# Performance work log

Measured on AMD Instinct MI355X. Metric: run time of the kernel, lower is better.

## Reference

```python
import jax, jax.numpy as jnp
import numpy as np

NDIM = 1024
NHEAD = 16
HEAD_DIM = NDIM // NHEAD


def setup_inputs() -> dict:
    key = jax.random.key(0)
    ks = jax.random.split(key, 12)
    B, L, C = 2, 2048, NDIM
    s = 0.02
    return {
        "q": jax.random.normal(ks[0], (B, L, C), jnp.float32),
        "k": jax.random.normal(ks[1], (B, L, C), jnp.float32),
        "v": jax.random.normal(ks[2], (B, L, C), jnp.float32),
        "Wq": jax.random.normal(ks[3], (C, C), jnp.float32) * s,
        "bq": jax.random.normal(ks[4], (C,), jnp.float32) * s,
        "Wk": jax.random.normal(ks[5], (C, C), jnp.float32) * s,
        "bk": jax.random.normal(ks[6], (C,), jnp.float32) * s,
        "Wv": jax.random.normal(ks[7], (C, C), jnp.float32) * s,
        "bv": jax.random.normal(ks[8], (C,), jnp.float32) * s,
        "Wo": jax.random.normal(ks[9], (C, C), jnp.float32) * s,
        "bo": jax.random.normal(ks[10], (C,), jnp.float32) * s,
    }


def reference(q, k, v, Wq, bq, Wk, bk, Wv, bv, Wo, bo):
    B, Lq, C = q.shape
    H, D = NHEAD, HEAD_DIM
    # projections, then split heads: (B, H, L, D)
    qh = (q @ Wq + bq).reshape(B, Lq, H, D).transpose(0, 2, 1, 3)
    kh = (k @ Wk + bk).reshape(B, k.shape[1], H, D).transpose(0, 2, 1, 3)
    vh = (v @ Wv + bv).reshape(B, v.shape[1], H, D).transpose(0, 2, 1, 3)
    scale = 1.0 / jnp.sqrt(jnp.asarray(D, qh.dtype))
    att = jnp.einsum("bhqd,bhkd->bhqk", qh, kh) * scale  # (B,H,Lq,Lk)
    att = jax.nn.softmax(att, axis=-1)  # dropout p=0.0 -> identity
    y = jnp.einsum("bhqk,bhkd->bhqd", att, vh)
    y = y.transpose(0, 2, 1, 3).reshape(B, Lq, C)
    return y @ Wo + bo
```

## Files before the change

### kernel.cpp

```cpp
#include <hip/hip_runtime.h>
#include <math.h>

#define BATCH 2
#define SEQ   2048
#define CDIM  1024
#define NHEAD 16
#define HDIM  64
#define TOKS  (BATCH * SEQ)

typedef __bf16 bf16x8 __attribute__((ext_vector_type(8)));
typedef __bf16 bf16x2 __attribute__((ext_vector_type(2)));
typedef float  f32x4  __attribute__((ext_vector_type(4)));
typedef float  f32x16 __attribute__((ext_vector_type(16)));

#define MFMA16(a, b, c) __builtin_amdgcn_mfma_f32_16x16x32_bf16(a, b, c, 0, 0, 0)
#define MFMA32(a, b, c) __builtin_amdgcn_mfma_f32_32x32x16_bf16(a, b, c, 0, 0, 0)

#define QSCALE 0.1803368801111204f

__device__ __forceinline__ void gload_lds16(const __bf16* g, __bf16* l) {
    __builtin_amdgcn_global_load_lds(
        (const __attribute__((address_space(1))) unsigned int*)g,
        (__attribute__((address_space(3))) unsigned int*)l, 16, 0, 0);
}

__global__ __launch_bounds__(256) void prep_kernel(
    const float* __restrict__ q, const float* __restrict__ k, const float* __restrict__ v,
    __bf16* __restrict__ qo, __bf16* __restrict__ ko, __bf16* __restrict__ vo,
    const float* __restrict__ W0, const float* __restrict__ W1,
    const float* __restrict__ W2, const float* __restrict__ W3,
    __bf16* __restrict__ T0, __bf16* __restrict__ T1,
    __bf16* __restrict__ T2, __bf16* __restrict__ T3)
{
    __shared__ __bf16 Ts[64][72];
    const int bx = blockIdx.x;
    const int tid = threadIdx.x;

    if (bx < 6144) {
        const int t = bx >> 11;
        const size_t i = ((size_t)(bx & 2047) * 256 + tid) * 8;
        const float* s = t == 0 ? q : (t == 1 ? k : v);
        __bf16* d = t == 0 ? qo : (t == 1 ? ko : vo);
        const float4 x = *(const float4*)&s[i];
        const float4 y = *(const float4*)&s[i + 4];
        bf16x8 o;
        o[0] = (__bf16)x.x; o[1] = (__bf16)x.y; o[2] = (__bf16)x.z; o[3] = (__bf16)x.w;
        o[4] = (__bf16)y.x; o[5] = (__bf16)y.y; o[6] = (__bf16)y.z; o[7] = (__bf16)y.w;
        *(bf16x8*)&d[i] = o;
        return;
    }

    const int t  = bx - 6144;
    const int z  = t >> 8;
    const int ry = (t & 255) >> 4;
    const int rx = t & 15;
    const float* W = z == 0 ? W0 : z == 1 ? W1 : z == 2 ? W2 : W3;
    __bf16* T = z == 0 ? T0 : z == 1 ? T1 : z == 2 ? T2 : T3;
    const int rb = ry * 64, cb = rx * 64;
    const int r = tid >> 4;
    const int c4 = (tid & 15) * 4;
#pragma unroll
    for (int p = 0; p < 4; p++) {
        const int rr = p * 16 + r;
        const float4 w4 = *(const float4*)&W[(size_t)(rb + rr) * CDIM + cb + c4];
        Ts[c4 + 0][rr] = (__bf16)w4.x;
        Ts[c4 + 1][rr] = (__bf16)w4.y;
        Ts[c4 + 2][rr] = (__bf16)w4.z;
        Ts[c4 + 3][rr] = (__bf16)w4.w;
    }
    __syncthreads();
    const int n = tid >> 2;
    const int k16 = (tid & 3) * 16;
    *(bf16x8*)&T[(size_t)(cb + n) * CDIM + rb + k16]     = *(const bf16x8*)&Ts[n][k16];
    *(bf16x8*)&T[(size_t)(cb + n) * CDIM + rb + k16 + 8] = *(const bf16x8*)&Ts[n][k16 + 8];
}

__global__ __launch_bounds__(512, 6) void qkv_gemm_kernel(
    const __bf16* __restrict__ qb, const __bf16* __restrict__ kb,
    const __bf16* __restrict__ vb,
    const __bf16* __restrict__ Wqt, const __bf16* __restrict__ Wkt,
    const __bf16* __restrict__ Wvt,
    const float* __restrict__ bq, const float* __restrict__ bk,
    const float* __restrict__ bv,
    __bf16* __restrict__ Qh, __bf16* __restrict__ Kh, __bf16* __restrict__ Vht)
{
    __shared__ __bf16 As[128 * 32];
    __shared__ __bf16 Bs[128 * 32];

    const int lin = blockIdx.x + (blockIdx.y << 3) + (blockIdx.z << 8);
    const int nl  = (lin & 7) * 96 + (lin >> 3);
    const int bx  = nl & 7;
    const int by  = (nl >> 3) & 31;
    const int z   = nl >> 8;

    const __bf16* A    = z == 0 ? qb : z == 1 ? kb : Wvt;
    const __bf16* Bt   = z == 0 ? Wqt : z == 1 ? Wkt : vb;
    const float*  bias = z == 0 ? bq : z == 1 ? bk : bv;

    const int tid  = threadIdx.x;
    const int w    = tid >> 6;
    const int lane = tid & 63;
    const int quad = lane >> 4;
    const int c    = lane & 15;
    const int wm   = w >> 1;
    const int wn   = w & 1;
    const int rowBase = (z == 2 ? bx : by) * 128;
    const int colBase = (z == 2 ? by : bx) * 128;

    const int sr = lane >> 2;
    const int sk = (lane & 3) * 8;

    f32x4 acc[2][4];
#pragma unroll
    for (int i = 0; i < 2; i++)
#pragma unroll
        for (int j = 0; j < 4; j++) acc[i][j] = (f32x4){0, 0, 0, 0};

    const __bf16* srcA = A  + (size_t)(rowBase + w * 16 + sr) * CDIM + sk;
    const __bf16* srcB = Bt + (size_t)(colBase + w * 16 + sr) * CDIM + sk;
    __bf16* dstA = &As[w * 16 * 32];
    __bf16* dstB = &Bs[w * 16 * 32];

    for (int k0 = 0; k0 < CDIM; k0 += 32) {
        gload_lds16(srcA + k0, dstA);
        gload_lds16(srcB + k0, dstB);
        __syncthreads();

        bf16x8 af[2], bf[4];
#pragma unroll
        for (int i = 0; i < 2; i++)
            af[i] = *(const bf16x8*)&As[(wm * 32 + i * 16 + c) * 32 + quad * 8];
#pragma unroll
        for (int i = 0; i < 4; i++)
            bf[i] = *(const bf16x8*)&Bs[(wn * 64 + i * 16 + c) * 32 + quad * 8];
#pragma unroll
        for (int mi = 0; mi < 2; mi++)
#pragma unroll
            for (int ni = 0; ni < 4; ni++)
                acc[mi][ni] = MFMA16(af[mi], bf[ni], acc[mi][ni]);
        __syncthreads();
    }

#pragma unroll
    for (int mi = 0; mi < 2; mi++) {
#pragma unroll
        for (int ni = 0; ni < 4; ni++) {
            const int col = colBase + wn * 64 + ni * 16 + c;
#pragma unroll
            for (int r = 0; r < 4; r++) {
                const int row = rowBase + wm * 32 + mi * 16 + quad * 4 + r;
                const float val = acc[mi][ni][r];
                if (z == 2) {
                    Vht[(size_t)row * TOKS + col] = (__bf16)(val + bias[row]);
                } else {
                    const int b = row >> 11, l = row & 2047;
                    const int h = col >> 6,  d = col & 63;
                    const float s = (z == 0) ? QSCALE : 1.0f;
                    __bf16* outp = (z == 0) ? Qh : Kh;
                    outp[((((size_t)b * NHEAD + h) * SEQ) + l) * HDIM + d] =
                        (__bf16)((val + bias[col]) * s);
                }
            }
        }
    }
}

__global__ __launch_bounds__(512, 4) void out_gemm_kernel(
    const __bf16* __restrict__ A, const __bf16* __restrict__ Bt,
    const float* __restrict__ bias, float* __restrict__ out)
{
    __shared__ __bf16 As[128 * 32];
    __shared__ __bf16 Bs[64 * 32];

    const int lin = blockIdx.x + (blockIdx.y << 4);
    const int nl  = (lin & 7) * 64 + (lin >> 3);
    const int bx  = nl & 15;
    const int by  = nl >> 4;

    const int tid  = threadIdx.x;
    const int w    = tid >> 6;
    const int lane = tid & 63;
    const int quad = lane >> 4;
    const int c    = lane & 15;
    const int wm   = w >> 1;
    const int wn   = w & 1;
    const int rowBase = by * 128;
    const int colBase = bx * 64;
    const int sr = lane >> 2;
    const int sk = (lane & 3) * 8;

    f32x4 acc[2][2];
#pragma unroll
    for (int i = 0; i < 2; i++)
#pragma unroll
        for (int j = 0; j < 2; j++) acc[i][j] = (f32x4){0, 0, 0, 0};

    const __bf16* srcA = A + (size_t)(rowBase + w * 16 + sr) * CDIM + sk;
    const __bf16* srcB = Bt + (size_t)(colBase + (w & 3) * 16 + sr) * CDIM + sk;
    __bf16* dstA = &As[w * 16 * 32];
    __bf16* dstB = &Bs[(w & 3) * 16 * 32];

    for (int k0 = 0; k0 < CDIM; k0 += 32) {
        gload_lds16(srcA + k0, dstA);
        if (w < 4) gload_lds16(srcB + k0, dstB);
        __syncthreads();

        bf16x8 af[2], bf[2];
#pragma unroll
        for (int i = 0; i < 2; i++)
            af[i] = *(const bf16x8*)&As[(wm * 32 + i * 16 + c) * 32 + quad * 8];
#pragma unroll
        for (int i = 0; i < 2; i++)
            bf[i] = *(const bf16x8*)&Bs[(wn * 32 + i * 16 + c) * 32 + quad * 8];
#pragma unroll
        for (int mi = 0; mi < 2; mi++)
#pragma unroll
            for (int ni = 0; ni < 2; ni++)
                acc[mi][ni] = MFMA16(af[mi], bf[ni], acc[mi][ni]);
        __syncthreads();
    }

#pragma unroll
    for (int mi = 0; mi < 2; mi++) {
#pragma unroll
        for (int ni = 0; ni < 2; ni++) {
            const int col = colBase + wn * 32 + ni * 16 + c;
#pragma unroll
            for (int r = 0; r < 4; r++) {
                const int row = rowBase + wm * 32 + mi * 16 + quad * 4 + r;
                out[(size_t)row * CDIM + col] = acc[mi][ni][r] + bias[col];
            }
        }
    }
}

__global__ __launch_bounds__(256, 2) void attn_v7_kernel(
    const __bf16* __restrict__ Qh, const __bf16* __restrict__ Kh,
    const __bf16* __restrict__ Vht, __bf16* __restrict__ Y)
{
    __shared__ __align__(16) __bf16 Ks[2][64][72];
    __shared__ __align__(16) __bf16 Vt[2][64][72];

    const int tid  = threadIdx.x;
    const int w    = tid >> 6;
    const int lane = tid & 63;
    const int l31  = lane & 31;
    const int hi   = lane >> 5;
    const int bh   = blockIdx.x;
    const int b    = bh >> 4;
    const int h    = bh & 15;
    const int qbase = blockIdx.y * 128 + w * 32;

    const __bf16* Qg = Qh + (size_t)bh * SEQ * HDIM;
    const __bf16* Kg = Kh + (size_t)bh * SEQ * HDIM;
    const __bf16* Vg = Vht + (size_t)(h * HDIM) * TOKS + (size_t)b * SEQ;

    bf16x8 qf[4];
#pragma unroll
    for (int ks = 0; ks < 4; ks++)
        qf[ks] = *(const bf16x8*)&Qg[(size_t)(qbase + l31) * HDIM + ks * 16 + hi * 8];

    f32x16 O[2];
#pragma unroll
    for (int i = 0; i < 2; i++)
#pragma unroll
        for (int j = 0; j < 16; j++) O[i][j] = 0.0f;
    float Lp = 0.0f;

    const int srow = tid >> 2;
    const int scol = (tid & 3) * 16;

    *(bf16x8*)&Ks[0][srow][scol]     = *(const bf16x8*)&Kg[(size_t)srow * HDIM + scol];
    *(bf16x8*)&Ks[0][srow][scol + 8] = *(const bf16x8*)&Kg[(size_t)srow * HDIM + scol + 8];
    *(bf16x8*)&Vt[0][srow][scol]     = *(const bf16x8*)&Vg[(size_t)srow * TOKS + scol];
    *(bf16x8*)&Vt[0][srow][scol + 8] = *(const bf16x8*)&Vg[(size_t)srow * TOKS + scol + 8];
    __syncthreads();

    int buf = 0;
    for (int t0 = 0; t0 < SEQ; t0 += 64) {
        const int tn = t0 + 64;
        bf16x8 kp0, kp1, vp0, vp1;
        if (tn < SEQ) {
            kp0 = *(const bf16x8*)&Kg[(size_t)(tn + srow) * HDIM + scol];
            kp1 = *(const bf16x8*)&Kg[(size_t)(tn + srow) * HDIM + scol + 8];
            vp0 = *(const bf16x8*)&Vg[(size_t)srow * TOKS + tn + scol];
            vp1 = *(const bf16x8*)&Vg[(size_t)srow * TOKS + tn + scol + 8];
        }

#pragma unroll
        for (int kt = 0; kt < 2; kt++) {
            f32x16 st;
#pragma unroll
            for (int j = 0; j < 16; j++) st[j] = 0.0f;
            __builtin_amdgcn_s_setprio(1);
#pragma unroll
            for (int ks = 0; ks < 4; ks++) {
                const bf16x8 kf =
                    *(const bf16x8*)&Ks[buf][kt * 32 + l31][ks * 16 + hi * 8];
                st = MFMA32(kf, qf[ks], st);
            }
            __builtin_amdgcn_s_setprio(0);

            float p[16];
#pragma unroll
            for (int j = 0; j < 16; j++) p[j] = __builtin_amdgcn_exp2f(st[j]);

#pragma unroll
            for (int kl = 0; kl < 2; kl++) {
                const int r0 = kl * 8;
                union { bf16x2 v; unsigned int u; } pa, pb, pc, pd;
                pa.v[0] = (__bf16)p[r0 + 0]; pa.v[1] = (__bf16)p[r0 + 1];
                pb.v[0] = (__bf16)p[r0 + 2]; pb.v[1] = (__bf16)p[r0 + 3];
                pc.v[0] = (__bf16)p[r0 + 4]; pc.v[1] = (__bf16)p[r0 + 5];
                pd.v[0] = (__bf16)p[r0 + 6]; pd.v[1] = (__bf16)p[r0 + 7];
                Lp += (float)pa.v[0] + (float)pa.v[1] + (float)pb.v[0] + (float)pb.v[1]
                    + (float)pc.v[0] + (float)pc.v[1] + (float)pd.v[0] + (float)pd.v[1];
                const unsigned int ax = __shfl_xor(pa.u, 32);
                const unsigned int bx = __shfl_xor(pb.u, 32);
                const unsigned int cx = __shfl_xor(pc.u, 32);
                const unsigned int dx = __shfl_xor(pd.u, 32);
                union { unsigned int u[4]; bf16x8 v; } af;
                af.u[0] = hi ? cx : pa.u;
                af.u[1] = hi ? dx : pb.u;
                af.u[2] = hi ? pc.u : ax;
                af.u[3] = hi ? pd.u : bx;
                const int kcol = kt * 32 + kl * 16 + hi * 8;
                __builtin_amdgcn_s_setprio(1);
#pragma unroll
                for (int dt = 0; dt < 2; dt++) {
                    const bf16x8 vf =
                        *(const bf16x8*)&Vt[buf][dt * 32 + l31][kcol];
                    O[dt] = MFMA32(af.v, vf, O[dt]);
                }
                __builtin_amdgcn_s_setprio(0);
            }
        }

        if (tn < SEQ) {
            *(bf16x8*)&Ks[buf ^ 1][srow][scol]     = kp0;
            *(bf16x8*)&Ks[buf ^ 1][srow][scol + 8] = kp1;
            *(bf16x8*)&Vt[buf ^ 1][srow][scol]     = vp0;
            *(bf16x8*)&Vt[buf ^ 1][srow][scol + 8] = vp1;
        }
        __syncthreads();
        buf ^= 1;
    }

    const float Lt  = Lp + __shfl_xor(Lp, 32);
    const float inv = 1.0f / Lt;

    __bf16* Yb = Y + (size_t)b * SEQ * CDIM;
#pragma unroll
    for (int reg = 0; reg < 16; reg++) {
        const int qrow  = (reg & 3) + 8 * (reg >> 2) + 4 * hi;
        const float iq  = __shfl(inv, qrow);
        __bf16* yp = Yb + (size_t)(qbase + qrow) * CDIM + h * HDIM + l31;
        yp[0]  = (__bf16)(O[0][reg] * iq);
        yp[32] = (__bf16)(O[1][reg] * iq);
    }
}


extern "C" void kernel_launch(void* const* d_in, const int* in_sizes, int n_in,
                              void* d_out, int out_size, void* d_ws, size_t ws_size,
                              hipStream_t stream)
{
    const float* q  = (const float*)d_in[0];
    const float* k  = (const float*)d_in[1];
    const float* v  = (const float*)d_in[2];
    const float* Wq = (const float*)d_in[3];
    const float* bq = (const float*)d_in[4];
    const float* Wk = (const float*)d_in[5];
    const float* bk = (const float*)d_in[6];
    const float* Wv = (const float*)d_in[7];
    const float* bv = (const float*)d_in[8];
    const float* Wo = (const float*)d_in[9];
    const float* bo = (const float*)d_in[10];
    float* out = (float*)d_out;

    const size_t MAT = (size_t)TOKS * CDIM;
    const size_t WN  = (size_t)CDIM * CDIM;

    __bf16* p   = (__bf16*)d_ws;
    __bf16* qb  = p; p += MAT;
    __bf16* kb  = p; p += MAT;
    __bf16* vb  = p; p += MAT;
    __bf16* Wqt = p; p += WN;
    __bf16* Wkt = p; p += WN;
    __bf16* Wvt = p; p += WN;
    __bf16* Wot = p; p += WN;
    __bf16* Qh  = p; p += MAT;
    __bf16* Kh  = p; p += MAT;
    __bf16* Vht = p; p += MAT;
    __bf16* Yb  = qb;

    prep_kernel<<<dim3(7168), dim3(256), 0, stream>>>(
        q, k, v, qb, kb, vb, Wq, Wk, Wv, Wo, Wqt, Wkt, Wvt, Wot);

    qkv_gemm_kernel<<<dim3(8, 32, 3), dim3(512), 0, stream>>>(
        qb, kb, vb, Wqt, Wkt, Wvt, bq, bk, bv, Qh, Kh, Vht);

    attn_v7_kernel<<<dim3(BATCH * NHEAD, SEQ / 128), dim3(256), 0, stream>>>(Qh, Kh, Vht, Yb);

    out_gemm_kernel<<<dim3(16, 32), dim3(512), 0, stream>>>(Yb, Wot, bo, out);
}
```

Baseline: 227.2 us.

## Compute softmax row sums via MFMA with ones, use permlane32 swap

```diff
diff --git a/kernel.cpp b/kernel.cpp
--- a/kernel.cpp
+++ b/kernel.cpp
@@ -234,7 +234,7 @@
     }
 }
 
-__global__ __launch_bounds__(256, 2) void attn_v7_kernel(
+__global__ __launch_bounds__(256, 2) void attn_v8_kernel(
     const __bf16* __restrict__ Qh, const __bf16* __restrict__ Kh,
     const __bf16* __restrict__ Vht, __bf16* __restrict__ Y)
 {
@@ -260,12 +260,13 @@
     for (int ks = 0; ks < 4; ks++)
         qf[ks] = *(const bf16x8*)&Qg[(size_t)(qbase + l31) * HDIM + ks * 16 + hi * 8];
 
-    f32x16 O[2];
-#pragma unroll
-    for (int i = 0; i < 2; i++)
-#pragma unroll
-        for (int j = 0; j < 16; j++) O[i][j] = 0.0f;
-    float Lp = 0.0f;
+    bf16x8 ones;
+#pragma unroll
+    for (int j = 0; j < 8; j++) ones[j] = (__bf16)1.0f;
+
+    f32x16 O[2], LA;
+#pragma unroll
+    for (int j = 0; j < 16; j++) { O[0][j] = 0.0f; O[1][j] = 0.0f; LA[j] = 0.0f; }
 
     const int srow = tid >> 2;
     const int scol = (tid & 3) * 16;
@@ -289,21 +290,22 @@
 
 #pragma unroll
         for (int kt = 0; kt < 2; kt++) {
-            f32x16 st;
-#pragma unroll
-            for (int j = 0; j < 16; j++) st[j] = 0.0f;
-            __builtin_amdgcn_s_setprio(1);
-#pragma unroll
-            for (int ks = 0; ks < 4; ks++) {
-                const bf16x8 kf =
-                    *(const bf16x8*)&Ks[buf][kt * 32 + l31][ks * 16 + hi * 8];
-                st = MFMA32(kf, qf[ks], st);
-            }
-            __builtin_amdgcn_s_setprio(0);
+            f32x16 st0, st1;
+#pragma unroll
+            for (int j = 0; j < 16; j++) { st0[j] = 0.0f; st1[j] = 0.0f; }
+            const bf16x8 kf0 = *(const bf16x8*)&Ks[buf][kt * 32 + l31][hi * 8];
+            const bf16x8 kf1 = *(const bf16x8*)&Ks[buf][kt * 32 + l31][16 + hi * 8];
+            const bf16x8 kf2 = *(const bf16x8*)&Ks[buf][kt * 32 + l31][32 + hi * 8];
+            const bf16x8 kf3 = *(const bf16x8*)&Ks[buf][kt * 32 + l31][48 + hi * 8];
+            st0 = MFMA32(kf0, qf[0], st0);
+            st1 = MFMA32(kf1, qf[1], st1);
+            st0 = MFMA32(kf2, qf[2], st0);
+            st1 = MFMA32(kf3, qf[3], st1);
 
             float p[16];
 #pragma unroll
-            for (int j = 0; j < 16; j++) p[j] = __builtin_amdgcn_exp2f(st[j]);
+            for (int j = 0; j < 16; j++)
+                p[j] = __builtin_amdgcn_exp2f(st0[j] + st1[j]);
 
 #pragma unroll
             for (int kl = 0; kl < 2; kl++) {
@@ -313,19 +315,15 @@
                 pb.v[0] = (__bf16)p[r0 + 2]; pb.v[1] = (__bf16)p[r0 + 3];
                 pc.v[0] = (__bf16)p[r0 + 4]; pc.v[1] = (__bf16)p[r0 + 5];
                 pd.v[0] = (__bf16)p[r0 + 6]; pd.v[1] = (__bf16)p[r0 + 7];
-                Lp += (float)pa.v[0] + (float)pa.v[1] + (float)pb.v[0] + (float)pb.v[1]
-                    + (float)pc.v[0] + (float)pc.v[1] + (float)pd.v[0] + (float)pd.v[1];
-                const unsigned int ax = __shfl_xor(pa.u, 32);
-                const unsigned int bx = __shfl_xor(pb.u, 32);
-                const unsigned int cx = __shfl_xor(pc.u, 32);
-                const unsigned int dx = __shfl_xor(pd.u, 32);
+                asm volatile("v_permlane32_swap_b32 %0, %1"
+                             : "+v"(pa.u), "+v"(pc.u));
+                asm volatile("v_permlane32_swap_b32 %0, %1"
+                             : "+v"(pb.u), "+v"(pd.u));
                 union { unsigned int u[4]; bf16x8 v; } af;
-                af.u[0] = hi ? cx : pa.u;
-                af.u[1] = hi ? dx : pb.u;
-                af.u[2] = hi ? pc.u : ax;
-                af.u[3] = hi ? pd.u : bx;
+                af.u[0] = pa.u; af.u[1] = pb.u; af.u[2] = pc.u; af.u[3] = pd.u;
                 const int kcol = kt * 32 + kl * 16 + hi * 8;
                 __builtin_amdgcn_s_setprio(1);
+                LA = MFMA32(af.v, ones, LA);
 #pragma unroll
                 for (int dt = 0; dt < 2; dt++) {
                     const bf16x8 vf =
@@ -346,14 +344,11 @@
         buf ^= 1;
     }
 
-    const float Lt  = Lp + __shfl_xor(Lp, 32);
-    const float inv = 1.0f / Lt;
-
     __bf16* Yb = Y + (size_t)b * SEQ * CDIM;
 #pragma unroll
     for (int reg = 0; reg < 16; reg++) {
         const int qrow  = (reg & 3) + 8 * (reg >> 2) + 4 * hi;
-        const float iq  = __shfl(inv, qrow);
+        const float iq  = 1.0f / LA[reg];
         __bf16* yp = Yb + (size_t)(qbase + qrow) * CDIM + h * HDIM + l31;
         yp[0]  = (__bf16)(O[0][reg] * iq);
         yp[32] = (__bf16)(O[1][reg] * iq);
@@ -400,7 +395,7 @@
     qkv_gemm_kernel<<<dim3(8, 32, 3), dim3(512), 0, stream>>>(
         qb, kb, vb, Wqt, Wkt, Wvt, bq, bk, bv, Qh, Kh, Vht);
 
-    attn_v7_kernel<<<dim3(BATCH * NHEAD, SEQ / 128), dim3(256), 0, stream>>>(Qh, Kh, Vht, Yb);
+    attn_v8_kernel<<<dim3(BATCH * NHEAD, SEQ / 128), dim3(256), 0, stream>>>(Qh, Kh, Vht, Yb);
 
     out_gemm_kernel<<<dim3(16, 32), dim3(512), 0, stream>>>(Yb, Wot, bo, out);
 }
```

Measured after the change: 218.2 us. 3.9% less time.
